# Kernel tuning notes

Measured on AMD Instinct MI355X. Metric: run time of the kernel, lower is better.

The kernel has to match this reference:

```python
import jax, jax.numpy as jnp
import numpy as np

B, S, E, H = 4, 2048, 2048, 16
D = E // H  # head_dim = 128
ROPE_BASE = 10000.0


def rope(x, base=ROPE_BASE, offset=0):
    # x: (..., seq, d) with interleaved even/odd rotation
    d = x.shape[-1]
    s = x.shape[-2]
    inv_freq = base ** (-jnp.arange(0, d, 2, dtype=jnp.float32) / d)  # (d/2,)
    pos = jnp.arange(offset, s + offset, dtype=jnp.float32)  # (s,)
    ang = pos[:, None] * inv_freq  # (s, d/2)
    sin, cos = jnp.sin(ang), jnp.cos(ang)
    xe, xo = x[..., 0::2], x[..., 1::2]
    re = xe * cos - xo * sin
    ro = xe * sin + xo * cos
    return jnp.stack([re, ro], axis=-1).reshape(x.shape)


def setup_inputs() -> dict:
    key = jax.random.key(0)
    ks = jax.random.split(key, 9)
    w = lambda k, shp: jax.random.normal(k, shp, dtype=jnp.float32) * 0.02
    return {
        "x": jax.random.normal(ks[0], (B, S, E), dtype=jnp.float32),
        "Wq": w(ks[1], (E, E)), "bq": w(ks[2], (E,)),
        "Wk": w(ks[3], (E, E)), "bk": w(ks[4], (E,)),
        "Wv": w(ks[5], (E, E)), "bv": w(ks[6], (E,)),
        "Wo": w(ks[7], (E, E)), "bo": w(ks[8], (E,)),
    }


def reference(x, Wq, bq, Wk, bk, Wv, bv, Wo, bo):
    b, s, _ = x.shape
    scale = D ** -0.5
    # torch Linear: y = x @ W.T + b
    def proj(W, bias):
        y = jnp.einsum('bse,fe->bsf', x, W) + bias
        return y.reshape(b, s, H, D).transpose(0, 2, 1, 3)  # (b, h, s, d)
    q = rope(proj(Wq, bq))
    k = rope(proj(Wk, bk))
    v = proj(Wv, bv)
    attn = jnp.einsum('bhqd,bhkd->bhqk', q, k) * scale  # (b, h, s, s)
    causal = jnp.triu(jnp.ones((s, s), dtype=bool), k=1)
    attn = jnp.where(causal, -jnp.inf, attn)
    attn_weights = jax.nn.softmax(attn, axis=-1)
    out = jnp.einsum('bhqk,bhkd->bhqd', attn_weights, v)
    out = out.transpose(0, 2, 1, 3).reshape(b, s, E)
    return jnp.einsum('bse,fe->bsf', out, Wo) + bo
```

## Files before the change

### kernel.cpp

```cpp
#include <hip/hip_runtime.h>
#include <hip/hip_bf16.h>
#include <stdint.h>

#define B_ 4
#define S_ 2048
#define E_ 2048
#define H_ 16
#define D_ 128
#define M_ (B_ * S_)

typedef unsigned short ushort_t;
typedef unsigned int uint_t;
typedef __attribute__((ext_vector_type(4))) float f32x4;
typedef __attribute__((ext_vector_type(2))) uint_t u32x2;
typedef __attribute__((ext_vector_type(8))) short bf16x8;

__device__ __forceinline__ ushort_t f2bf(float f) {
  uint_t u = __float_as_uint(f);
  u += 0x7FFFu + ((u >> 16) & 1u);
  return (ushort_t)(u >> 16);
}
__device__ __forceinline__ float bf2f(ushort_t h) {
  return __uint_as_float(((uint_t)h) << 16);
}
__device__ __forceinline__ uint_t cvt_pk_bf16(float lo, float hi) {
  uint_t r;
  asm("v_cvt_pk_bf16_f32 %0, %1, %2" : "=v"(r) : "v"(lo), "v"(hi));
  return r;
}

#define GLOAD_LDS16(gp, lp)                                   \
  __builtin_amdgcn_global_load_lds(                           \
      (__attribute__((address_space(1))) void*)(gp),          \
      (__attribute__((address_space(3))) void*)(lp), 16, 0, 0)

__global__ void f32_to_bf16(const float* __restrict__ in, ushort_t* __restrict__ out,
                            size_t n4) {
  const size_t stride = (size_t)gridDim.x * blockDim.x;
  for (size_t i = (size_t)blockIdx.x * blockDim.x + threadIdx.x; i < n4; i += stride) {
    const f32x4 f = __builtin_nontemporal_load((const f32x4*)in + i);
    u32x2 o;
    o[0] = (uint_t)f2bf(f[0]) | ((uint_t)f2bf(f[1]) << 16);
    o[1] = (uint_t)f2bf(f[2]) | ((uint_t)f2bf(f[3]) << 16);
    __builtin_nontemporal_store(o, (u32x2*)out + i);
  }
}

template <int MODE>
__global__ __launch_bounds__(512, 1) void gemm256(const ushort_t* __restrict__ A,
                                                  const ushort_t* __restrict__ Bw,
                                                  const float* __restrict__ bias,
                                                  void* __restrict__ Cv) {
  __shared__ __align__(16) char lds[135168];
  const int tid = threadIdx.x;
  const int w = tid >> 6, l = tid & 63, g = l >> 4, ln = l & 15;
  const int wm = w >> 2, wn = w & 3;

  const int flat = blockIdx.x;
  const int swz = (flat & 7) * 32 + (flat >> 3);
  const int m0 = (swz >> 3) * 256, n0 = (swz & 7) * 256;

  const ushort_t* Ab = A + (size_t)m0 * E_;
  const ushort_t* Bb = Bw + (size_t)n0 * E_;

  int srcRow[2], srcCc[2];
#pragma unroll
  for (int i = 0; i < 2; i++) {
    const int c = i * 512 + tid;
    const int r2 = c >> 3;
    const int j = (c & 7) ^ (r2 & 7);
    srcRow[i] = 2 * r2 + (j >> 2);
    srcCc[i] = (j & 3) * 8;
  }

  const int NT = E_ / 64;

  auto STAGE = [&](int t_, int mat, int kk) {
    char* dst = lds + (t_ & 1) * 65536 + mat * 32768 + kk * 16384;
    const ushort_t* src = mat ? Bb : Ab;
#pragma unroll
    for (int i = 0; i < 2; i++)
      GLOAD_LDS16(src + (size_t)srcRow[i] * E_ + t_ * 64 + kk * 32 + srcCc[i],
                  dst + (i * 512 + w * 64) * 16);
  };

  const int rp = ln >> 1;
  const int chunkl = ((((ln & 1) << 2) | g) ^ rp);
  const int aBase = wm * 8192 + rp * 128 + chunkl * 16;
  const int bBase = 32768 + wn * 4096 + rp * 128 + chunkl * 16;

  f32x4 acc[8][4];
#pragma unroll
  for (int mi = 0; mi < 8; mi++)
#pragma unroll
    for (int ni = 0; ni < 4; ni++)
#pragma unroll
      for (int r = 0; r < 4; r++) acc[mi][ni][r] = 0.f;

  STAGE(0, 0, 0);
  STAGE(0, 1, 0);
  STAGE(0, 0, 1);
  STAGE(0, 1, 1);

  for (int t = 0; t < NT; t++) {
    const char* bp = lds + (t & 1) * 65536;
    const bool nxt = (t + 1 < NT);
    bf16x8 bfr[4], af[4];

    asm volatile("s_waitcnt vmcnt(4)" ::: "memory");
    __builtin_amdgcn_s_barrier();
#pragma unroll
    for (int ni = 0; ni < 4; ni++) bfr[ni] = *(const bf16x8*)(bp + bBase + ni * 1024);
#pragma unroll
    for (int ai = 0; ai < 4; ai++) af[ai] = *(const bf16x8*)(bp + aBase + ai * 1024);
    if (nxt) STAGE(t + 1, 0, 0);
    asm volatile("s_waitcnt lgkmcnt(0)" ::: "memory");
    __builtin_amdgcn_sched_barrier(0);
    __builtin_amdgcn_s_setprio(1);
#pragma unroll
    for (int ai = 0; ai < 4; ai++)
#pragma unroll
      for (int ni = 0; ni < 4; ni++)
        acc[ai][ni] = __builtin_amdgcn_mfma_f32_16x16x32_bf16(af[ai], bfr[ni], acc[ai][ni], 0, 0, 0);
    __builtin_amdgcn_s_setprio(0);

    __builtin_amdgcn_s_barrier();
#pragma unroll
    for (int ai = 0; ai < 4; ai++) af[ai] = *(const bf16x8*)(bp + aBase + 4096 + ai * 1024);
    if (nxt) STAGE(t + 1, 1, 0);
    asm volatile("s_waitcnt lgkmcnt(0)" ::: "memory");
    __builtin_amdgcn_sched_barrier(0);
    __builtin_amdgcn_s_setprio(1);
#pragma unroll
    for (int ai = 0; ai < 4; ai++)
#pragma unroll
      for (int ni = 0; ni < 4; ni++)
        acc[4 + ai][ni] =
            __builtin_amdgcn_mfma_f32_16x16x32_bf16(af[ai], bfr[ni], acc[4 + ai][ni], 0, 0, 0);
    __builtin_amdgcn_s_setprio(0);

    if (nxt)
      asm volatile("s_waitcnt vmcnt(4)" ::: "memory");
    else
      asm volatile("s_waitcnt vmcnt(0)" ::: "memory");
    __builtin_amdgcn_s_barrier();
#pragma unroll
    for (int ni = 0; ni < 4; ni++) bfr[ni] = *(const bf16x8*)(bp + bBase + 16384 + ni * 1024);
#pragma unroll
    for (int ai = 0; ai < 4; ai++) af[ai] = *(const bf16x8*)(bp + aBase + 16384 + ai * 1024);
    if (nxt) STAGE(t + 1, 0, 1);
    asm volatile("s_waitcnt lgkmcnt(0)" ::: "memory");
    __builtin_amdgcn_sched_barrier(0);
    __builtin_amdgcn_s_setprio(1);
#pragma unroll
    for (int ai = 0; ai < 4; ai++)
#pragma unroll
      for (int ni = 0; ni < 4; ni++)
        acc[ai][ni] = __builtin_amdgcn_mfma_f32_16x16x32_bf16(af[ai], bfr[ni], acc[ai][ni], 0, 0, 0);
    __builtin_amdgcn_s_setprio(0);

    __builtin_amdgcn_s_barrier();
#pragma unroll
    for (int ai = 0; ai < 4; ai++)
      af[ai] = *(const bf16x8*)(bp + aBase + 16384 + 4096 + ai * 1024);
    if (nxt) STAGE(t + 1, 1, 1);
    asm volatile("s_waitcnt lgkmcnt(0)" ::: "memory");
    __builtin_amdgcn_sched_barrier(0);
    __builtin_amdgcn_s_setprio(1);
#pragma unroll
    for (int ai = 0; ai < 4; ai++)
#pragma unroll
      for (int ni = 0; ni < 4; ni++)
        acc[4 + ai][ni] =
            __builtin_amdgcn_mfma_f32_16x16x32_bf16(af[ai], bfr[ni], acc[4 + ai][ni], 0, 0, 0);
    __builtin_amdgcn_s_setprio(0);
  }

  float bv[4];
#pragma unroll
  for (int ni = 0; ni < 4; ni++) bv[ni] = bias[n0 + wn * 64 + ni * 16 + ln];

#pragma unroll
  for (int mh = 0; mh < 2; mh++) {
    __builtin_amdgcn_s_barrier();
    if (MODE == 3) {
      float* Ct = (float*)lds;
#pragma unroll
      for (int ai = 0; ai < 4; ai++)
#pragma unroll
        for (int ni = 0; ni < 4; ni++) {
          const int col = wn * 64 + ni * 16 + ln;
          const int rr = wm * 64 + ai * 16 + g * 4;
          f32x4 v = acc[mh * 4 + ai][ni];
#pragma unroll
          for (int r = 0; r < 4; r++) v[r] += bv[ni];
          *(f32x4*)(Ct + col * 132 + rr) = v;
        }
      __builtin_amdgcn_s_barrier();
#pragma unroll
      for (int i = 0; i < 16; i++) {
        const int c = i * 512 + tid;
        const int rq = c & 31, cl = c >> 5;
        const f32x4 v = *(const f32x4*)((const float*)lds + cl * 132 + rq * 4);
        const int gcol = n0 + cl;
        const int hh = gcol >> 7, d = gcol & 127;
        const int bb = m0 >> 11;
        const int s = (m0 & (S_ - 1)) + (rq >> 4) * 128 + mh * 64 + (rq & 15) * 4;
        *(uint2*)((ushort_t*)Cv + (((size_t)(bb * H_ + hh) * D_ + d) * S_ + s)) =
            make_uint2(cvt_pk_bf16(v[0], v[1]), cvt_pk_bf16(v[2], v[3]));
      }
    } else {
      float* Cl = (float*)lds;
#pragma unroll
      for (int ai = 0; ai < 4; ai++)
#pragma unroll
        for (int ni = 0; ni < 4; ni++) {
          const int col = wn * 64 + ni * 16 + ln;
          const int rr0 = wm * 64 + ai * 16 + g * 4;
#pragma unroll
          for (int r = 0; r < 4; r++)
            Cl[(rr0 + r) * 260 + col] = acc[mh * 4 + ai][ni][r] + bv[ni];
        }
      __builtin_amdgcn_s_barrier();
#pragma unroll
      for (int i = 0; i < 16; i++) {
        const int c = i * 512 + tid;
        const int chk = c & 63, rr = c >> 6;
        const f32x4 v = *(const f32x4*)((const float*)lds + rr * 260 + chk * 4);
        const int grow = m0 + (rr >> 6) * 128 + mh * 64 + (rr & 63);
        const int gcol = n0 + chk * 4;
        if (MODE == 1) {
          __builtin_nontemporal_store(v, (f32x4*)((float*)Cv + (size_t)grow * E_ + gcol));
        } else {
          const int s = grow & (S_ - 1);
          const int ip0 = (gcol & 127) >> 1;
          float sn0, cs0, sn1, cs1;
          sincosf((float)s * exp2f(-0.20762050593046f * (float)ip0), &sn0, &cs0);
          sincosf((float)s * exp2f(-0.20762050593046f * (float)(ip0 + 1)), &sn1, &cs1);
          const float re0 = v[0] * cs0 - v[1] * sn0, ro0 = v[0] * sn0 + v[1] * cs0;
          const float re1 = v[2] * cs1 - v[3] * sn1, ro1 = v[2] * sn1 + v[3] * cs1;
          *(uint2*)((ushort_t*)Cv + (size_t)grow * E_ + gcol) =
              make_uint2(cvt_pk_bf16(re0, ro0), cvt_pk_bf16(re1, ro1));
        }
      }
    }
  }
}

__global__ __launch_bounds__(256, 2) void attn_fwd(const ushort_t* __restrict__ Q,
                                                   const ushort_t* __restrict__ K,
                                                   const ushort_t* __restrict__ Vt,
                                                   ushort_t* __restrict__ O) {
  const int flat = blockIdx.x;
  const int pair = flat >> 6;
  const int bh = flat & 63;
  const int b = bh >> 4, h = bh & 15;
  const int tid = threadIdx.x;
  const int w = tid >> 6, l = tid & 63, g = l >> 4, ln = l & 15;

  __shared__ ushort_t Ks[2][64 * 128];
  __shared__ ushort_t Vs[2][128 * 64];
  __shared__ ushort_t Ps[4][32 * 64];

  const ushort_t* Kb = K + (size_t)(b * S_) * E_ + h * D_;
  const ushort_t* Vb = Vt + (size_t)(b * H_ + h) * D_ * S_;
  const float scale = 0.08838834764831845f;

#define STAGE_KV(buf, kv0_)                                                      \
  do {                                                                           \
    _Pragma("unroll") for (int i = 0; i < 4; i++) {                              \
      const int c = i * 256 + tid;                                               \
      const int row = c >> 4, sl = c & 15;                                       \
      const int gs = sl ^ (row & 7);                                             \
      GLOAD_LDS16(Kb + (size_t)((kv0_) + row) * E_ + gs * 8,                     \
                  (char*)(&Ks[buf][0]) + (i * 256 + w * 64) * 16);               \
    }                                                                            \
    _Pragma("unroll") for (int i = 0; i < 4; i++) {                              \
      const int c = i * 256 + tid;                                               \
      const int row = c >> 3, sl = c & 7;                                        \
      const int gs = sl ^ (row & 7);                                             \
      GLOAD_LDS16(Vb + (size_t)row * S_ + (kv0_) + gs * 8,                       \
                  (char*)(&Vs[buf][0]) + (i * 256 + w * 64) * 16);               \
    }                                                                            \
  } while (0)

  for (int pass = 0; pass < 2; pass++) {
    const int u = (pass == 0) ? pair : (15 - pair);
    const int q0 = u * 128;
    const int wrow0 = q0 + w * 32;

    bf16x8 qf[2][4];
    {
      const ushort_t* qb = Q + (size_t)(b * S_ + wrow0) * E_ + h * D_;
#pragma unroll
      for (int mi = 0; mi < 2; mi++)
#pragma unroll
        for (int kk = 0; kk < 4; kk++) {
          bf16x8 v = *(const bf16x8*)(qb + (size_t)(mi * 16 + ln) * E_ + kk * 32 + g * 8);
#pragma unroll
          for (int j = 0; j < 8; j++) v[j] = (short)f2bf(bf2f((ushort_t)v[j]) * scale);
          qf[mi][kk] = v;
        }
    }

    f32x4 oacc[2][8];
#pragma unroll
    for (int mi = 0; mi < 2; mi++)
#pragma unroll
      for (int nd = 0; nd < 8; nd++)
#pragma unroll
        for (int r = 0; r < 4; r++) oacc[mi][nd][r] = 0.f;
    float mrun[2], srun[2];
#pragma unroll
    for (int mi = 0; mi < 2; mi++) {
      mrun[mi] = -__builtin_inff();
      srun[mi] = 0.f;
    }

    const int ntu = 2 * u + 2;
    STAGE_KV(0, 0);

    for (int t = 0; t < ntu; t++) {
      const int kv0 = t * 64;
      const int cur = t & 1;
      if (t + 1 < ntu) {
        STAGE_KV(cur ^ 1, kv0 + 64);
        asm volatile("s_waitcnt vmcnt(8)" ::: "memory");
      } else {
        asm volatile("s_waitcnt vmcnt(0)" ::: "memory");
      }
      __builtin_amdgcn_s_barrier();
      __builtin_amdgcn_sched_barrier(0);

      if (kv0 <= wrow0 + 31) {
        const ushort_t* Kst = &Ks[cur][0];
        const ushort_t* Vst = &Vs[cur][0];
        f32x4 sa[2][4];
#pragma unroll
        for (int mi = 0; mi < 2; mi++)
#pragma unroll
          for (int ni = 0; ni < 4; ni++)
#pragma unroll
            for (int r = 0; r < 4; r++) sa[mi][ni][r] = 0.f;
        __builtin_amdgcn_s_setprio(1);
#pragma unroll
        for (int kk = 0; kk < 4; kk++) {
          bf16x8 kf[4];
#pragma unroll
          for (int ni = 0; ni < 4; ni++) {
            const int row = ni * 16 + ln;
            const int sl = (kk * 4 + g) ^ (row & 7);
            kf[ni] = *(const bf16x8*)(Kst + row * 128 + sl * 8);
          }
#pragma unroll
          for (int mi = 0; mi < 2; mi++)
#pragma unroll
            for (int ni = 0; ni < 4; ni++)
              sa[mi][ni] =
                  __builtin_amdgcn_mfma_f32_16x16x32_bf16(kf[ni], qf[mi][kk], sa[mi][ni], 0, 0, 0);
        }
        __builtin_amdgcn_s_setprio(0);
        if (kv0 + 63 > wrow0) {
#pragma unroll
          for (int mi = 0; mi < 2; mi++) {
            const int lim = wrow0 + mi * 16 + ln - kv0;
#pragma unroll
            for (int ni = 0; ni < 4; ni++)
#pragma unroll
              for (int r = 0; r < 4; r++)
                if (ni * 16 + g * 4 + r > lim) sa[mi][ni][r] = -__builtin_inff();
          }
        }
#pragma unroll
        for (int mi = 0; mi < 2; mi++) {
          float vmax = -__builtin_inff();
#pragma unroll
          for (int ni = 0; ni < 4; ni++)
#pragma unroll
            for (int r = 0; r < 4; r++) vmax = fmaxf(vmax, sa[mi][ni][r]);
          vmax = fmaxf(vmax, __shfl_xor(vmax, 16));
          vmax = fmaxf(vmax, __shfl_xor(vmax, 32));
          if (!__all(vmax - mrun[mi] <= 8.0f)) {
            const float mnew = fmaxf(mrun[mi], vmax);
            const float fs = __expf(mrun[mi] - mnew);
            mrun[mi] = mnew;
            srun[mi] *= fs;
#pragma unroll
            for (int nd = 0; nd < 8; nd++)
#pragma unroll
              for (int r = 0; r < 4; r++) oacc[mi][nd][r] *= fs;
          }
          const float m = mrun[mi];
          float psum = 0.f;
#pragma unroll
          for (int ni = 0; ni < 4; ni++) {
            float p0 = __expf(sa[mi][ni][0] - m);
            float p1 = __expf(sa[mi][ni][1] - m);
            float p2 = __expf(sa[mi][ni][2] - m);
            float p3 = __expf(sa[mi][ni][3] - m);
            psum += (p0 + p1) + (p2 + p3);
            const int byteW =
                (((mi * 16 + ln) * 64 + ni * 16 + g * 4) * 2) ^ ((ln & 7) << 4);
            *(uint2*)((char*)(&Ps[w][0]) + byteW) =
                make_uint2(cvt_pk_bf16(p0, p1), cvt_pk_bf16(p2, p3));
          }
          psum += __shfl_xor(psum, 16);
          psum += __shfl_xor(psum, 32);
          srun[mi] += psum;
        }
        asm volatile("s_waitcnt lgkmcnt(0)" ::: "memory");
        __builtin_amdgcn_sched_barrier(0);
        __builtin_amdgcn_s_setprio(1);
#pragma unroll
        for (int ks = 0; ks < 2; ks++) {
          bf16x8 pf[2];
#pragma unroll
          for (int mi = 0; mi < 2; mi++) {
            const int byteR =
                (((mi * 16 + ln) * 64 + ks * 32 + g * 8) * 2) ^ ((ln & 7) << 4);
            pf[mi] = *(const bf16x8*)((const char*)(&Ps[w][0]) + byteR);
          }
#pragma unroll
          for (int nd = 0; nd < 8; nd++) {
            const int row = nd * 16 + ln;
            const int sl = (ks * 4 + g) ^ (row & 7);
            const bf16x8 vf = *(const bf16x8*)(Vst + row * 64 + sl * 8);
#pragma unroll
            for (int mi = 0; mi < 2; mi++)
              oacc[mi][nd] =
                  __builtin_amdgcn_mfma_f32_16x16x32_bf16(vf, pf[mi], oacc[mi][nd], 0, 0, 0);
          }
        }
        __builtin_amdgcn_s_setprio(0);
      }
      __builtin_amdgcn_s_barrier();
    }

    {
      ushort_t* Ob = O + (size_t)(b * S_ + q0 + w * 32) * E_ + h * D_;
#pragma unroll
      for (int mi = 0; mi < 2; mi++) {
        const float inv = 1.0f / srun[mi];
#pragma unroll
        for (int nd = 0; nd < 8; nd++) {
          const uint_t lo = cvt_pk_bf16(oacc[mi][nd][0] * inv, oacc[mi][nd][1] * inv);
          const uint_t hi = cvt_pk_bf16(oacc[mi][nd][2] * inv, oacc[mi][nd][3] * inv);
          *(uint2*)(Ob + (size_t)(mi * 16 + ln) * E_ + nd * 16 + g * 4) = make_uint2(lo, hi);
        }
      }
    }
  }
#undef STAGE_KV
}

extern "C" void kernel_launch(void* const* d_in, const int* in_sizes, int n_in,
                              void* d_out, int out_size, void* d_ws, size_t ws_size,
                              hipStream_t stream) {
  const float* x = (const float*)d_in[0];
  const float* Wq = (const float*)d_in[1];
  const float* bq = (const float*)d_in[2];
  const float* Wk = (const float*)d_in[3];
  const float* bk = (const float*)d_in[4];
  const float* Wv = (const float*)d_in[5];
  const float* bv = (const float*)d_in[6];
  const float* Wo = (const float*)d_in[7];
  const float* bo = (const float*)d_in[8];
  float* out = (float*)d_out;

  ushort_t* ws = (ushort_t*)d_ws;
  const size_t SZ = (size_t)M_ * E_;
  const size_t WSZ = (size_t)E_ * E_;
  ushort_t* xb = ws;
  ushort_t* Qb = ws + SZ;
  ushort_t* Kb = ws + 2 * SZ;
  ushort_t* Vtb = ws + 4 * SZ;
  ushort_t* Wqb = ws + 5 * SZ;
  ushort_t* Wkb = Wqb + WSZ;
  ushort_t* Wvb = Wkb + WSZ;
  ushort_t* Wob = Wvb + WSZ;
  ushort_t* Ob = xb;

  f32_to_bf16<<<2048, 256, 0, stream>>>(x, xb, SZ / 4);
  f32_to_bf16<<<1024, 256, 0, stream>>>(Wq, Wqb, WSZ / 4);
  f32_to_bf16<<<1024, 256, 0, stream>>>(Wk, Wkb, WSZ / 4);
  f32_to_bf16<<<1024, 256, 0, stream>>>(Wv, Wvb, WSZ / 4);
  f32_to_bf16<<<1024, 256, 0, stream>>>(Wo, Wob, WSZ / 4);

  gemm256<2><<<256, 512, 0, stream>>>(xb, Wqb, bq, Qb);
  gemm256<2><<<256, 512, 0, stream>>>(xb, Wkb, bk, Kb);
  gemm256<3><<<256, 512, 0, stream>>>(xb, Wvb, bv, Vtb);

  attn_fwd<<<512, 256, 0, stream>>>(Qb, Kb, Vtb, Ob);

  gemm256<1><<<256, 512, 0, stream>>>(Ob, Wob, bo, (void*)out);
}
```

Baseline: 496.3 us.

## Replace projection GEMMs with simple 128-tile kernel, rope table, separate V transpose

Adds a new 128x128 single-buffered GEMM kernel (gemm_bt) that writes results straight from registers, and uses it for the Q, V and output projections. The 256-tile pipelined kernel is kept only for K, and its staged LDS epilogue is replaced by direct per-element stores. RoPE sin/cos now come from a precomputed table instead of sincosf per element. V is transposed by a separate kernel rather than in the GEMM epilogue. The simpler kernel gives up the double-buffered prefetch pipeline, and the direct 2-byte scattered stores are uncoalesced, so both GEMM throughput and store efficiency are at risk.

```diff
diff --git a/kernel.cpp b/kernel.cpp
--- a/kernel.cpp
+++ b/kernel.cpp
@@ -46,12 +46,134 @@
   }
 }
 
+__global__ void rope_table(float2* __restrict__ tab) {
+  const int i = blockIdx.x * 256 + threadIdx.x;
+  const int s = i >> 6, p = i & 63;
+  const float inv = exp2f(-0.20762050593046f * (float)p);
+  float sn, cs;
+  sincosf((float)s * inv, &sn, &cs);
+  tab[i] = make_float2(cs, sn);
+}
+
+__global__ __launch_bounds__(256) void transpose_v(const ushort_t* __restrict__ Vp,
+                                                   ushort_t* __restrict__ Vt) {
+  const int b = blockIdx.z, h = blockIdx.y;
+  const int s0 = blockIdx.x * 64;
+  const int tid = threadIdx.x;
+  __shared__ ushort_t T[64][136];
+#pragma unroll
+  for (int i = 0; i < 4; i++) {
+    const int c = i * 256 + tid;
+    const int s = c >> 4, d8 = c & 15;
+    *(bf16x8*)(&T[s][d8 * 8]) =
+        *(const bf16x8*)(Vp + (size_t)(b * S_ + s0 + s) * E_ + h * D_ + d8 * 8);
+  }
+  __syncthreads();
+#pragma unroll
+  for (int i = 0; i < 4; i++) {
+    const int c = i * 256 + tid;
+    const int d = c >> 3, s8 = c & 7;
+    bf16x8 v;
+#pragma unroll
+    for (int j = 0; j < 8; j++) v[j] = (short)T[s8 * 8 + j][d];
+    *(bf16x8*)(Vt + ((size_t)(b * H_ + h) * D_ + d) * S_ + s0 + s8 * 8) = v;
+  }
+}
+
 template <int MODE>
-__global__ __launch_bounds__(512, 1) void gemm256(const ushort_t* __restrict__ A,
+__global__ __launch_bounds__(256, 2) void gemm_bt(const ushort_t* __restrict__ A,
                                                   const ushort_t* __restrict__ Bw,
                                                   const float* __restrict__ bias,
+                                                  const float2* __restrict__ tab,
                                                   void* __restrict__ Cv) {
-  __shared__ __align__(16) char lds[135168];
+  __shared__ ushort_t As[128 * 64];
+  __shared__ ushort_t Bs[128 * 64];
+  const int tid = threadIdx.x;
+  const int w = tid >> 6, l = tid & 63, g = l >> 4, ln = l & 15;
+  const int wm = w >> 1, wn = w & 1;
+  const int flat = blockIdx.y * 16 + blockIdx.x;
+  const int swz = (flat & 7) * 128 + (flat >> 3);
+  const int m0 = (swz >> 4) * 128, n0 = (swz & 15) * 128;
+
+  f32x4 acc[4][4];
+#pragma unroll
+  for (int i = 0; i < 4; i++)
+#pragma unroll
+    for (int j = 0; j < 4; j++)
+#pragma unroll
+      for (int r = 0; r < 4; r++) acc[i][j][r] = 0.f;
+
+  const ushort_t* Ab = A + (size_t)m0 * E_;
+  const ushort_t* Bb = Bw + (size_t)n0 * E_;
+
+  for (int k0 = 0; k0 < E_; k0 += 64) {
+    __syncthreads();
+#pragma unroll
+    for (int i = 0; i < 4; i++) {
+      const int c = i * 256 + tid;
+      const int row = c >> 3;
+      const int gs = (c & 7) ^ (row & 7);
+      GLOAD_LDS16(Ab + (size_t)row * E_ + k0 + gs * 8, (char*)As + (i * 256 + w * 64) * 16);
+      GLOAD_LDS16(Bb + (size_t)row * E_ + k0 + gs * 8, (char*)Bs + (i * 256 + w * 64) * 16);
+    }
+    __syncthreads();
+#pragma unroll
+    for (int kk = 0; kk < 2; kk++) {
+      bf16x8 af[4], bfr[4];
+#pragma unroll
+      for (int mi = 0; mi < 4; mi++) {
+        const int row = wm * 64 + mi * 16 + ln;
+        const int sl = (kk * 4 + g) ^ (row & 7);
+        af[mi] = *(const bf16x8*)(As + row * 64 + sl * 8);
+      }
+#pragma unroll
+      for (int ni = 0; ni < 4; ni++) {
+        const int row = wn * 64 + ni * 16 + ln;
+        const int sl = (kk * 4 + g) ^ (row & 7);
+        bfr[ni] = *(const bf16x8*)(Bs + row * 64 + sl * 8);
+      }
+#pragma unroll
+      for (int mi = 0; mi < 4; mi++)
+#pragma unroll
+        for (int ni = 0; ni < 4; ni++)
+          acc[mi][ni] =
+              __builtin_amdgcn_mfma_f32_16x16x32_bf16(af[mi], bfr[ni], acc[mi][ni], 0, 0, 0);
+    }
+  }
+
+  float bv[4];
+#pragma unroll
+  for (int ni = 0; ni < 4; ni++) bv[ni] = bias[n0 + wn * 64 + ni * 16 + ln];
+#pragma unroll
+  for (int mi = 0; mi < 4; mi++)
+#pragma unroll
+    for (int ni = 0; ni < 4; ni++) {
+      const int col = n0 + wn * 64 + ni * 16 + ln;
+      const int p = (col & 127) >> 1;
+      const float sgn = (col & 1) ? 1.f : -1.f;
+#pragma unroll
+      for (int r = 0; r < 4; r++) {
+        const float v = acc[mi][ni][r] + bv[ni];
+        const size_t row = m0 + wm * 64 + mi * 16 + g * 4 + r;
+        if (MODE == 1) {
+          ((float*)Cv)[row * E_ + col] = v;
+        } else if (MODE == 2) {
+          const float partner = __shfl_xor(v, 1);
+          const float2 t = tab[(row & (S_ - 1)) * 64 + p];
+          ((ushort_t*)Cv)[row * E_ + col] = f2bf(v * t.x + sgn * partner * t.y);
+        } else {
+          ((ushort_t*)Cv)[row * E_ + col] = f2bf(v);
+        }
+      }
+    }
+}
+
+__global__ __launch_bounds__(512, 2) void gemm_k256(const ushort_t* __restrict__ A,
+                                                    const ushort_t* __restrict__ Bw,
+                                                    const float* __restrict__ bias,
+                                                    const float2* __restrict__ tab,
+                                                    ushort_t* __restrict__ Cv) {
+  __shared__ __align__(16) char lds[131072];
   const int tid = threadIdx.x;
   const int w = tid >> 6, l = tid & 63, g = l >> 4, ln = l & 15;
   const int wm = w >> 2, wn = w & 3;
@@ -107,7 +229,10 @@
     const bool nxt = (t + 1 < NT);
     bf16x8 bfr[4], af[4];
 
-    asm volatile("s_waitcnt vmcnt(4)" ::: "memory");
+    if (nxt)
+      asm volatile("s_waitcnt vmcnt(4)" ::: "memory");
+    else
+      asm volatile("s_waitcnt vmcnt(0)" ::: "memory");
     __builtin_amdgcn_s_barrier();
 #pragma unroll
     for (int ni = 0; ni < 4; ni++) bfr[ni] = *(const bf16x8*)(bp + bBase + ni * 1024);
@@ -179,72 +304,22 @@
   float bv[4];
 #pragma unroll
   for (int ni = 0; ni < 4; ni++) bv[ni] = bias[n0 + wn * 64 + ni * 16 + ln];
-
-#pragma unroll
-  for (int mh = 0; mh < 2; mh++) {
-    __builtin_amdgcn_s_barrier();
-    if (MODE == 3) {
-      float* Ct = (float*)lds;
-#pragma unroll
-      for (int ai = 0; ai < 4; ai++)
-#pragma unroll
-        for (int ni = 0; ni < 4; ni++) {
-          const int col = wn * 64 + ni * 16 + ln;
-          const int rr = wm * 64 + ai * 16 + g * 4;
-          f32x4 v = acc[mh * 4 + ai][ni];
-#pragma unroll
-          for (int r = 0; r < 4; r++) v[r] += bv[ni];
-          *(f32x4*)(Ct + col * 132 + rr) = v;
-        }
-      __builtin_amdgcn_s_barrier();
-#pragma unroll
-      for (int i = 0; i < 16; i++) {
-        const int c = i * 512 + tid;
-        const int rq = c & 31, cl = c >> 5;
-        const f32x4 v = *(const f32x4*)((const float*)lds + cl * 132 + rq * 4);
-        const int gcol = n0 + cl;
-        const int hh = gcol >> 7, d = gcol & 127;
-        const int bb = m0 >> 11;
-        const int s = (m0 & (S_ - 1)) + (rq >> 4) * 128 + mh * 64 + (rq & 15) * 4;
-        *(uint2*)((ushort_t*)Cv + (((size_t)(bb * H_ + hh) * D_ + d) * S_ + s)) =
-            make_uint2(cvt_pk_bf16(v[0], v[1]), cvt_pk_bf16(v[2], v[3]));
-      }
-    } else {
-      float* Cl = (float*)lds;
-#pragma unroll
-      for (int ai = 0; ai < 4; ai++)
-#pragma unroll
-        for (int ni = 0; ni < 4; ni++) {
-          const int col = wn * 64 + ni * 16 + ln;
-          const int rr0 = wm * 64 + ai * 16 + g * 4;
-#pragma unroll
-          for (int r = 0; r < 4; r++)
-            Cl[(rr0 + r) * 260 + col] = acc[mh * 4 + ai][ni][r] + bv[ni];
-        }
-      __builtin_amdgcn_s_barrier();
-#pragma unroll
-      for (int i = 0; i < 16; i++) {
-        const int c = i * 512 + tid;
-        const int chk = c & 63, rr = c >> 6;
-        const f32x4 v = *(const f32x4*)((const float*)lds + rr * 260 + chk * 4);
-        const int grow = m0 + (rr >> 6) * 128 + mh * 64 + (rr & 63);
-        const int gcol = n0 + chk * 4;
-        if (MODE == 1) {
-          __builtin_nontemporal_store(v, (f32x4*)((float*)Cv + (size_t)grow * E_ + gcol));
-        } else {
-          const int s = grow & (S_ - 1);
-          const int ip0 = (gcol & 127) >> 1;
-          float sn0, cs0, sn1, cs1;
-          sincosf((float)s * exp2f(-0.20762050593046f * (float)ip0), &sn0, &cs0);
-          sincosf((float)s * exp2f(-0.20762050593046f * (float)(ip0 + 1)), &sn1, &cs1);
-          const float re0 = v[0] * cs0 - v[1] * sn0, ro0 = v[0] * sn0 + v[1] * cs0;
-          const float re1 = v[2] * cs1 - v[3] * sn1, ro1 = v[2] * sn1 + v[3] * cs1;
-          *(uint2*)((ushort_t*)Cv + (size_t)grow * E_ + gcol) =
-              make_uint2(cvt_pk_bf16(re0, ro0), cvt_pk_bf16(re1, ro1));
-        }
-      }
-    }
-  }
+#pragma unroll
+  for (int mi = 0; mi < 8; mi++)
+#pragma unroll
+    for (int ni = 0; ni < 4; ni++) {
+      const int col = n0 + wn * 64 + ni * 16 + ln;
+      const int p = (col & 127) >> 1;
+      const float sgn = (col & 1) ? 1.f : -1.f;
+      const int row0 = m0 + wm * 128 + mi * 16 + g * 4;
+#pragma unroll
+      for (int r = 0; r < 4; r++) {
+        const float v = acc[mi][ni][r] + bv[ni];
+        const float partner = __shfl_xor(v, 1);
+        const float2 t = tab[((row0 + r) & (S_ - 1)) * 64 + p];
+        Cv[(size_t)(row0 + r) * E_ + col] = f2bf(v * t.x + sgn * partner * t.y);
+      }
+    }
 }
 
 __global__ __launch_bounds__(256, 2) void attn_fwd(const ushort_t* __restrict__ Q,
@@ -473,6 +548,8 @@
   ushort_t* xb = ws;
   ushort_t* Qb = ws + SZ;
   ushort_t* Kb = ws + 2 * SZ;
+  float2* tbl = (float2*)(ws + 3 * SZ);
+  ushort_t* Vb = ws + 3 * SZ;
   ushort_t* Vtb = ws + 4 * SZ;
   ushort_t* Wqb = ws + 5 * SZ;
   ushort_t* Wkb = Wqb + WSZ;
@@ -485,12 +562,15 @@
   f32_to_bf16<<<1024, 256, 0, stream>>>(Wk, Wkb, WSZ / 4);
   f32_to_bf16<<<1024, 256, 0, stream>>>(Wv, Wvb, WSZ / 4);
   f32_to_bf16<<<1024, 256, 0, stream>>>(Wo, Wob, WSZ / 4);
-
-  gemm256<2><<<256, 512, 0, stream>>>(xb, Wqb, bq, Qb);
-  gemm256<2><<<256, 512, 0, stream>>>(xb, Wkb, bk, Kb);
-  gemm256<3><<<256, 512, 0, stream>>>(xb, Wvb, bv, Vtb);
+  rope_table<<<512, 256, 0, stream>>>(tbl);
+
+  dim3 gg(16, 64);
+  gemm_bt<2><<<gg, 256, 0, stream>>>(xb, Wqb, bq, tbl, Qb);
+  gemm_k256<<<256, 512, 0, stream>>>(xb, Wkb, bk, tbl, Kb);
+  gemm_bt<0><<<gg, 256, 0, stream>>>(xb, Wvb, bv, nullptr, Vb);
+  transpose_v<<<dim3(32, H_, B_), 256, 0, stream>>>(Vb, Vtb);
 
   attn_fwd<<<512, 256, 0, stream>>>(Qb, Kb, Vtb, Ob);
 
-  gemm256<1><<<256, 512, 0, stream>>>(Ob, Wob, bo, (void*)out);
-}
+  gemm_bt<1><<<gg, 256, 0, stream>>>(Ob, Wob, bo, nullptr, (void*)out);
+}
```

Result: faster. 447.6 us (-9.8%).
